# Optimization experiments

Hardware: AMD Instinct MI355X
Metric: run time of the kernel (lower is better)

## Reference

```python
import jax, jax.numpy as jnp
import numpy as np

B, S, E = 2, 2049, 512
H, WIN = 8, 1024
D = E // H


def setup_inputs() -> dict:
    key = jax.random.key(0)
    ks = jax.random.split(key, 11)
    sc = 0.02
    return {
        "x": jax.random.normal(ks[0], (B, S, E), dtype=jnp.float32),
        "Wq": jax.random.normal(ks[1], (E, E), dtype=jnp.float32) * sc,
        "bq": jnp.zeros((E,), dtype=jnp.float32),
        "Wk": jax.random.normal(ks[2], (E, E), dtype=jnp.float32) * sc,
        "bk": jnp.zeros((E,), dtype=jnp.float32),
        "Wv": jax.random.normal(ks[3], (E, E), dtype=jnp.float32) * sc,
        "bv": jnp.zeros((E,), dtype=jnp.float32),
        "Wo": jax.random.normal(ks[4], (E, E), dtype=jnp.float32) * sc,
        "bo": jnp.zeros((E,), dtype=jnp.float32),
        "w_gate": jax.random.normal(ks[5], (2 * E,), dtype=jnp.float32) * sc,
        "b_gate": jnp.zeros((), dtype=jnp.float32),
    }


def reference(x, Wq, bq, Wk, bk, Wv, bv, Wo, bo, w_gate, b_gate):
    scale = D ** -0.5
    q_flat = x @ Wq + bq  # [B,S,E]
    k_flat = x @ Wk + bk
    v_flat = x @ Wv + bv
    q = q_flat.reshape(B, S, H, D).transpose(0, 2, 1, 3)  # [B,H,S,D]
    k = k_flat.reshape(B, S, H, D).transpose(0, 2, 1, 3)
    v = v_flat.reshape(B, S, H, D).transpose(0, 2, 1, 3)

    scores = jnp.einsum("bhqd,bhkd->bhqk", q, k) * scale  # [B,H,S,S]

    # Gaussian positional bias: -0.5*|i-j|^2/sigma^2, sigma = window/2
    pos = jnp.arange(S)
    dist = jnp.abs(pos[:, None] - pos[None, :]).astype(jnp.float32)
    sigma = WIN / 2.0
    bias = -0.5 * dist ** 2 / (sigma ** 2)  # [S,S]
    scores = scores + bias[None, None]

    # Pairwise gate: sigmoid(concat(q_i,k_j) @ w + b) == sigmoid(q_i.wq + k_j.wk + b)
    gq = q_flat @ w_gate[:E]       # [B,S]
    gk = k_flat @ w_gate[E:]       # [B,S]
    gates = jax.nn.sigmoid(gq[:, :, None] + gk[:, None, :] + b_gate)  # [B,S,S]
    scores = scores * gates[:, None]  # broadcast over heads

    local_mask = jnp.where(dist <= WIN, 0.0, -jnp.inf).astype(jnp.float32)
    scores = scores + local_mask[None, None]

    attn = jax.nn.softmax(scores, axis=-1)
    out = jnp.einsum("bhqk,bhkd->bhqd", attn, v)  # [B,H,S,D]
    out = out.transpose(0, 2, 1, 3).reshape(B, S, E)
    return out @ Wo + bo
```

## Files before the change

### kernel.cpp

```cpp
#include <hip/hip_runtime.h>
#include <cstdint>
#include <cstddef>

#define B_ 2
#define S_ 2049
#define E_ 512
#define H_ 8
#define WIN_ 1024
#define MROWS (B_*S_)
#define SP_ 2176
#define GBUFN 4104
#define BHS_ (B_*H_*S_)

typedef unsigned short ushort_t;
typedef __attribute__((ext_vector_type(8))) short bf16x8;
typedef __attribute__((ext_vector_type(4))) float f32x4;

#define MFMA16(a,b,c) __builtin_amdgcn_mfma_f32_16x16x32_bf16(a,b,c,0,0,0)

__device__ __forceinline__ ushort_t f2bf(float f) {
  unsigned int u = __float_as_uint(f);
  u += 0x7fffu + ((u >> 16) & 1u);
  return (ushort_t)(u >> 16);
}
__device__ __forceinline__ float bf2f(ushort_t h) {
  return __uint_as_float(((unsigned int)h) << 16);
}

__global__ __launch_bounds__(256) void convert_w_kernel(
    const float* __restrict__ W0, const float* __restrict__ W1,
    const float* __restrict__ W2, const float* __restrict__ W3,
    ushort_t* __restrict__ Wt_all, ushort_t* __restrict__ WoHi,
    float* __restrict__ gacc)
{
  __shared__ float tile[32][33];
  int z = blockIdx.z;
  if (z == 3) {
    int gz = (blockIdx.x * 16 + blockIdx.y) * 256 + threadIdx.x;
    if (gz < 2 * GBUFN) gacc[gz] = 0.f;
  }
  const float* W = (z == 0) ? W0 : (z == 1) ? W1 : (z == 2) ? W2 : W3;
  int k0 = blockIdx.x * 32, n0 = blockIdx.y * 32;
  int r = threadIdx.x >> 5, c = threadIdx.x & 31;
#pragma unroll
  for (int i = 0; i < 4; ++i) {
    int rr = r + i * 8;
    tile[rr][c] = W[(size_t)(k0 + rr) * E_ + n0 + c];
  }
  __syncthreads();
#pragma unroll
  for (int i = 0; i < 4; ++i) {
    int rr = r + i * 8;
    float v = tile[c][rr];
    size_t dst = (size_t)(n0 + rr) * E_ + k0 + c;
    if (z < 3) Wt_all[(size_t)z * E_ * E_ + dst] = f2bf(v);
    else       WoHi[dst] = f2bf(v);
  }
}

__global__ __launch_bounds__(256) void gemm_qkv_kernel(
    const float* __restrict__ x, const ushort_t* __restrict__ Wt_all,
    const float* __restrict__ bq, const float* __restrict__ bk,
    const float* __restrict__ bv, const float* __restrict__ wg,
    ushort_t* __restrict__ qkb, ushort_t* __restrict__ vT,
    float* __restrict__ gacc)
{
  __shared__ __align__(16) ushort_t As[64][40];
  __shared__ __align__(16) ushort_t Bs[128][40];
  int tid = threadIdx.x;
  int lane = tid & 63, w = tid >> 6;
  int l15 = lane & 15, quad = lane >> 4;
  int wm = (w & 1) * 32, wn = (w >> 1) * 64;
  int z = blockIdx.z;
  const ushort_t* Wt = Wt_all + (size_t)z * E_ * E_;
  const float* bias = (z == 0) ? bq : (z == 1) ? bk : bv;
  int bt = blockIdx.x;
  int bg2 = bt / 33;
  int bm = (bt - bg2 * 33) * 64;
  int bn = blockIdx.y * 128;
  size_t rowbase = (size_t)bg2 * S_;

  int ar = tid >> 2, acq = (tid & 3) * 8;
  int ai = bm + ar; if (ai >= S_) ai = S_ - 1;
  const float* ap = x + (rowbase + ai) * E_ + acq;
  int br = tid >> 1, bcq = (tid & 1) * 16;
  const ushort_t* bp = Wt + (size_t)(bn + br) * E_ + bcq;

  const f32x4 fz = {0.f, 0.f, 0.f, 0.f};
  f32x4 acc[2][4];
#pragma unroll
  for (int mt = 0; mt < 2; ++mt)
#pragma unroll
    for (int nt = 0; nt < 4; ++nt) acc[mt][nt] = fz;

  float4 pa0 = *(const float4*)ap, pa1 = *(const float4*)(ap + 4);
  int4  pb0 = *(const int4*)bp,   pb1 = *(const int4*)(bp + 8);

  for (int k0 = 0; k0 < E_; k0 += 32) {
    __syncthreads();
    int kn = (k0 + 32 < E_) ? (k0 + 32) : k0;
    float4 na0 = *(const float4*)(ap + kn), na1 = *(const float4*)(ap + kn + 4);
    int4  nb0 = *(const int4*)(bp + kn),   nb1 = *(const int4*)(bp + kn + 8);
    union { int4 v; ushort_t u[8]; } cv;
    cv.u[0] = f2bf(pa0.x); cv.u[1] = f2bf(pa0.y); cv.u[2] = f2bf(pa0.z); cv.u[3] = f2bf(pa0.w);
    cv.u[4] = f2bf(pa1.x); cv.u[5] = f2bf(pa1.y); cv.u[6] = f2bf(pa1.z); cv.u[7] = f2bf(pa1.w);
    *(int4*)&As[ar][acq] = cv.v;
    *(int4*)&Bs[br][bcq] = pb0; *(int4*)&Bs[br][bcq + 8] = pb1;
    __syncthreads();
    bf16x8 a[2], bfr[4];
#pragma unroll
    for (int mt = 0; mt < 2; ++mt) a[mt] = *(const bf16x8*)&As[wm + mt * 16 + l15][quad * 8];
#pragma unroll
    for (int nt = 0; nt < 4; ++nt) bfr[nt] = *(const bf16x8*)&Bs[wn + nt * 16 + l15][quad * 8];
#pragma unroll
    for (int mt = 0; mt < 2; ++mt)
#pragma unroll
      for (int nt = 0; nt < 4; ++nt)
        acc[mt][nt] = MFMA16(a[mt], bfr[nt], acc[mt][nt]);
    pa0 = na0; pa1 = na1; pb0 = nb0; pb1 = nb1;
  }

  float bb[4];
#pragma unroll
  for (int nt = 0; nt < 4; ++nt) bb[nt] = bias[bn + wn + nt * 16 + l15];

  if (z < 2) {
    ushort_t* C = qkb + (size_t)z * MROWS * E_;
#pragma unroll
    for (int mt = 0; mt < 2; ++mt)
#pragma unroll
      for (int nt = 0; nt < 4; ++nt)
#pragma unroll
        for (int r = 0; r < 4; ++r) {
          int i = bm + wm + mt * 16 + quad * 4 + r;
          if (i < S_)
            C[(rowbase + i) * E_ + bn + wn + nt * 16 + l15] = f2bf(acc[mt][nt][r] + bb[nt]);
        }
    const float* wgp = wg + (size_t)z * E_;
    float wv[4];
#pragma unroll
    for (int nt = 0; nt < 4; ++nt) wv[nt] = wgp[bn + wn + nt * 16 + l15];
    float* gp = gacc + (size_t)z * GBUFN;
#pragma unroll
    for (int mt = 0; mt < 2; ++mt)
#pragma unroll
      for (int r = 0; r < 4; ++r) {
        float s = 0.f;
#pragma unroll
        for (int nt = 0; nt < 4; ++nt) s = fmaf(acc[mt][nt][r] + bb[nt], wv[nt], s);
        s += __shfl_xor(s, 1, 16); s += __shfl_xor(s, 2, 16);
        s += __shfl_xor(s, 4, 16); s += __shfl_xor(s, 8, 16);
        int i = bm + wm + mt * 16 + quad * 4 + r;
        if (l15 == 0 && i < S_) atomicAdd(&gp[rowbase + i], s);
      }
  } else {
    ushort_t* lt = &Bs[0][0];
    int ti = tid >> 2, tc = (tid & 3) * 16;
#pragma unroll
    for (int hh = 0; hh < 2; ++hh) {
      __syncthreads();
      if ((w >> 1) == hh) {
#pragma unroll
        for (int mt = 0; mt < 2; ++mt)
#pragma unroll
          for (int nt = 0; nt < 4; ++nt) {
            int d = nt * 16 + l15;
#pragma unroll
            for (int r = 0; r < 4; ++r) {
              int il = wm + mt * 16 + quad * 4 + r;
              lt[d * 72 + il] = f2bf(acc[mt][nt][r] + bb[nt]);
            }
          }
      }
      __syncthreads();
      int hg = (bn >> 6) + hh;
      union { int4 q[2]; ushort_t u[16]; } tv;
      tv.q[0] = *(const int4*)&lt[ti * 72 + tc];
      tv.q[1] = *(const int4*)&lt[ti * 72 + tc + 8];
      size_t vrow = ((size_t)(bg2 * H_ + hg) * 64 + ti) * SP_;
#pragma unroll
      for (int c8 = 0; c8 < 2; ++c8) {
        int i2 = bm + tc + c8 * 8;
        if (i2 + 7 < S_) {
          *(int4*)&vT[vrow + i2] = tv.q[c8];
        } else {
#pragma unroll
          for (int e = 0; e < 8; ++e)
            if (i2 + e < S_) vT[vrow + i2 + e] = tv.u[c8 * 8 + e];
        }
      }
    }
  }
}

__global__ __launch_bounds__(256) void attn_kernel(
    const ushort_t* __restrict__ qb, const ushort_t* __restrict__ kb,
    const ushort_t* __restrict__ vT, const float* __restrict__ gq_raw,
    const float* __restrict__ gk_raw, const float* __restrict__ bgate,
    float* __restrict__ Opart, float* __restrict__ Lpart)
{
  __shared__ __align__(16) ushort_t Ks[64][72];
  __shared__ __align__(16) ushort_t Vt[64][72];
  __shared__ __align__(16) ushort_t Ps[4][16][72];
  __shared__ float gbs[704];

  int tid = threadIdx.x;
  int lane = tid & 63, w = tid >> 6;
  int l15 = lane & 15, quad = lane >> 4;

  int sub = blockIdx.x % 48;
  int qidx = blockIdx.x / 48;
  int off = (qidx + 1) >> 1;
  int qt = 16 + ((qidx & 1) ? -off : off);
  int bh = sub & 15, third = sub >> 4;
  int h = bh & 7, b = bh >> 3;
  int i0 = qt * 64;
  const float coef = -0.5f / (512.f * 512.f);

  int i = i0 + w * 16 + l15;
  int ic = (i < S_) ? i : S_ - 1;
  bf16x8 qf0 = *(const bf16x8*)&qb[((size_t)(b * S_ + ic)) * E_ + h * 64 + quad * 8];
  bf16x8 qf1 = *(const bf16x8*)&qb[((size_t)(b * S_ + ic)) * E_ + h * 64 + 32 + quad * 8];
#pragma unroll
  for (int e = 0; e < 8; ++e) {
    qf0[e] = (short)f2bf(bf2f((ushort_t)qf0[e]) * 0.125f);
    qf1[e] = (short)f2bf(bf2f((ushort_t)qf1[e]) * 0.125f);
  }
  float av = __expf(-(gq_raw[b * S_ + ic] + bgate[0]));
  float fdi = (i < S_) ? (float)i : -1e5f;

  int jlo = i0 - WIN_; if (jlo < 0) jlo = 0;
  int jt_lo = jlo >> 6;
  int jhi = i0 + 63 + WIN_; if (jhi > S_ - 1) jhi = S_ - 1;
  int jt_hi = jhi >> 6;
  int L = jt_hi - jt_lo + 1;
  int n0 = (L + 2) / 3, n1 = (L + 1) / 3;
  int myLo = jt_lo + ((third == 0) ? 0 : (third == 1) ? n0 : n0 + n1);
  int cnt = (third == 0) ? n0 : (third == 1) ? n1 : L - n0 - n1;
  int myHi = myLo + cnt - 1;
  int jbase = myLo << 6;
  int nwin = cnt << 6;

  for (int tt = tid; tt < nwin; tt += 256) {
    int j = jbase + tt; int jc = (j < S_) ? j : S_ - 1;
    gbs[tt] = __expf(-gk_raw[b * S_ + jc]);
  }

  int srow = tid >> 2, scol = (tid & 3) * 16;
  const ushort_t* kb_base = kb + (size_t)b * S_ * E_ + h * 64 + scol;
  const ushort_t* vb_base = vT + ((size_t)(b * H_ + h) * 64 + srow) * SP_ + scol;

  int4 ka0, ka1, va0, va1;
  {
    int jc0 = jbase + srow; if (jc0 > S_ - 1) jc0 = S_ - 1;
    const int4* kp = (const int4*)(kb_base + (size_t)jc0 * E_);
    ka0 = kp[0]; ka1 = kp[1];
    const int4* vp = (const int4*)(vb_base + jbase);
    va0 = vp[0]; va1 = vp[1];
  }

  const f32x4 fz = {0.f, 0.f, 0.f, 0.f};
  f32x4 Ov[4] = {fz, fz, fz, fz};
  float l_run = 0.f;

  for (int jt = myLo; jt <= myHi; ++jt) {
    int j0 = jt << 6;
    __syncthreads();
    int jn = (jt < myHi) ? ((jt + 1) << 6) : j0;
    int jcn = jn + srow; if (jcn > S_ - 1) jcn = S_ - 1;
    const int4* kp = (const int4*)(kb_base + (size_t)jcn * E_);
    int4 nk0 = kp[0], nk1 = kp[1];
    const int4* vp = (const int4*)(vb_base + jn);
    int4 nv0 = vp[0], nv1 = vp[1];
    *(int4*)&Ks[srow][scol] = ka0; *(int4*)&Ks[srow][scol + 8] = ka1;
    *(int4*)&Vt[srow][scol] = va0; *(int4*)&Vt[srow][scol + 8] = va1;
    __syncthreads();

    f32x4 st[4];
#pragma unroll
    for (int nt = 0; nt < 4; ++nt) {
      bf16x8 kf0 = *(const bf16x8*)&Ks[nt * 16 + l15][quad * 8];
      bf16x8 kf1 = *(const bf16x8*)&Ks[nt * 16 + l15][32 + quad * 8];
      f32x4 s = MFMA16(kf0, qf0, fz);
      st[nt] = MFMA16(kf1, qf1, s);
    }

    bool full = ((j0 + 63 - i0) <= WIN_) && ((i0 + 63 - j0) <= WIN_)
                && (j0 + 63 < S_) && (i0 + 63 < S_);
    float ps = 0.f;
    float jq = (float)(j0 + quad * 4);
    if (full) {
#pragma unroll
      for (int nt = 0; nt < 4; ++nt) {
        f32x4 g4 = *(const f32x4*)&gbs[(j0 - jbase) + nt * 16 + quad * 4];
#pragma unroll
        for (int r = 0; r < 4; ++r) {
          float f = fdi - (jq + (float)(nt * 16 + r));
          float gate = __builtin_amdgcn_rcpf(fmaf(av, g4[r], 1.f));
          float p = __expf(fmaf(f * f, coef, st[nt][r]) * gate);
          st[nt][r] = p; ps += p;
        }
      }
    } else {
#pragma unroll
      for (int nt = 0; nt < 4; ++nt) {
        f32x4 g4 = *(const f32x4*)&gbs[(j0 - jbase) + nt * 16 + quad * 4];
#pragma unroll
        for (int r = 0; r < 4; ++r) {
          int j = j0 + nt * 16 + quad * 4 + r;
          float fj = (j < S_) ? (float)j : 1e5f;
          float f = fdi - fj;
          float gate = __builtin_amdgcn_rcpf(fmaf(av, g4[r], 1.f));
          float t = fmaf(f * f, coef, st[nt][r]) * gate;
          t = (__builtin_fabsf(f) <= 1024.f) ? t : -1e30f;
          float p = __expf(t);
          st[nt][r] = p; ps += p;
        }
      }
    }
    ps += __shfl_xor(ps, 16);
    ps += __shfl_xor(ps, 32);
    l_run += ps;

#pragma unroll
    for (int nt = 0; nt < 4; ++nt) {
      uint2 pk;
      pk.x = (unsigned int)f2bf(st[nt][0]) | ((unsigned int)f2bf(st[nt][1]) << 16);
      pk.y = (unsigned int)f2bf(st[nt][2]) | ((unsigned int)f2bf(st[nt][3]) << 16);
      *(uint2*)&Ps[w][l15][nt * 16 + quad * 4] = pk;
    }
    bf16x8 p0 = *(const bf16x8*)&Ps[w][l15][quad * 8];
    bf16x8 p1 = *(const bf16x8*)&Ps[w][l15][32 + quad * 8];
#pragma unroll
    for (int nt = 0; nt < 4; ++nt) {
      bf16x8 v0 = *(const bf16x8*)&Vt[nt * 16 + l15][quad * 8];
      bf16x8 v1 = *(const bf16x8*)&Vt[nt * 16 + l15][32 + quad * 8];
      Ov[nt] = MFMA16(p0, v0, Ov[nt]);
      Ov[nt] = MFMA16(p1, v1, Ov[nt]);
    }
    ka0 = nk0; ka1 = nk1; va0 = nv0; va1 = nv1;
  }

  if (lane < 16) {
    int irow = i0 + w * 16 + lane;
    if (irow < S_)
      Lpart[(size_t)third * BHS_ + (size_t)(b * H_ + h) * S_ + irow] = l_run;
  }
#pragma unroll
  for (int r = 0; r < 4; ++r) {
    int irow = i0 + w * 16 + quad * 4 + r;
    if (irow < S_) {
      size_t base = ((size_t)third * BHS_ + (size_t)(b * H_ + h) * S_ + irow) * 64;
#pragma unroll
      for (int nt = 0; nt < 4; ++nt)
        Opart[base + nt * 16 + l15] = Ov[nt][r];
    }
  }
}

__global__ __launch_bounds__(256) void gemm_out_kernel(
    const float* __restrict__ Opart, const float* __restrict__ Lpart,
    const ushort_t* __restrict__ Whi, const float* __restrict__ bias,
    float* __restrict__ C)
{
  __shared__ __align__(16) ushort_t AsH[64][40];
  __shared__ __align__(16) ushort_t AsL[64][40];
  __shared__ __align__(16) ushort_t BsW[64][40];
  __shared__ float invL[64][8];
  int tid = threadIdx.x;
  int lane = tid & 63, w = tid >> 6;
  int l15 = lane & 15, quad = lane >> 4;
  int bm = blockIdx.x * 64, bn = blockIdx.y * 64;

  for (int idx = tid; idx < 512; idx += 256) {
    int r = idx >> 3, hh = idx & 7;
    int m = bm + r; if (m >= MROWS) m = MROWS - 1;
    int b2 = (m >= S_) ? 1 : 0;
    int i = m - b2 * S_;
    size_t li = (size_t)(b2 * H_ + hh) * S_ + i;
    float l = Lpart[li] + Lpart[(size_t)BHS_ + li] + Lpart[2 * (size_t)BHS_ + li];
    invL[r][hh] = 1.f / l;
  }

  int sr = tid >> 2, scq = (tid & 3) * 8;
  int m = bm + sr; if (m >= MROWS) m = MROWS - 1;
  int b2 = (m >= S_) ? 1 : 0;
  int i = m - b2 * S_;
  size_t obase = (((size_t)(b2 * H_) * S_) + i) * 64;
  const ushort_t* bp = Whi + (size_t)(bn + sr) * E_ + scq;

  const f32x4 fz = {0.f, 0.f, 0.f, 0.f};
  f32x4 acc[4] = {fz, fz, fz, fz};
  const size_t TOFF = (size_t)BHS_ * 64;

  for (int k0 = 0; k0 < E_; k0 += 32) {
    __syncthreads();
    int e0 = k0 + scq;
    int h = e0 >> 6, d = e0 & 63;
    const float* op = Opart + obase + (size_t)h * (S_ * 64) + d;
    float4 a0 = *(const float4*)op;
    float4 a1 = *(const float4*)(op + 4);
    float4 q0 = *(const float4*)(op + TOFF);
    float4 q1 = *(const float4*)(op + TOFF + 4);
    float4 c0 = *(const float4*)(op + 2 * TOFF);
    float4 c1 = *(const float4*)(op + 2 * TOFF + 4);
    float sc = invL[sr][h];
    float o[8] = {(a0.x + q0.x + c0.x) * sc, (a0.y + q0.y + c0.y) * sc,
                  (a0.z + q0.z + c0.z) * sc, (a0.w + q0.w + c0.w) * sc,
                  (a1.x + q1.x + c1.x) * sc, (a1.y + q1.y + c1.y) * sc,
                  (a1.z + q1.z + c1.z) * sc, (a1.w + q1.w + c1.w) * sc};
    union { int4 v; ushort_t u[8]; } hi, lo;
#pragma unroll
    for (int e = 0; e < 8; ++e) {
      ushort_t hv = f2bf(o[e]);
      hi.u[e] = hv;
      lo.u[e] = f2bf(o[e] - bf2f(hv));
    }
    *(int4*)&AsH[sr][scq] = hi.v;
    *(int4*)&AsL[sr][scq] = lo.v;
    *(int4*)&BsW[sr][scq] = *(const int4*)(bp + k0);
    __syncthreads();
    bf16x8 ah = *(const bf16x8*)&AsH[w * 16 + l15][quad * 8];
    bf16x8 al = *(const bf16x8*)&AsL[w * 16 + l15][quad * 8];
#pragma unroll
    for (int nt = 0; nt < 4; ++nt) {
      bf16x8 bw = *(const bf16x8*)&BsW[nt * 16 + l15][quad * 8];
      acc[nt] = MFMA16(ah, bw, acc[nt]);
      acc[nt] = MFMA16(al, bw, acc[nt]);
    }
  }
#pragma unroll
  for (int nt = 0; nt < 4; ++nt) {
    float bb = bias[bn + nt * 16 + l15];
#pragma unroll
    for (int r = 0; r < 4; ++r) {
      int mm = bm + w * 16 + quad * 4 + r;
      if (mm < MROWS)
        C[(size_t)mm * E_ + bn + nt * 16 + l15] = acc[nt][r] + bb;
    }
  }
}

extern "C" void kernel_launch(void* const* d_in, const int* in_sizes, int n_in,
                              void* d_out, int out_size, void* d_ws, size_t ws_size,
                              hipStream_t stream) {
  const float* x  = (const float*)d_in[0];
  const float* Wq = (const float*)d_in[1];
  const float* bq = (const float*)d_in[2];
  const float* Wk = (const float*)d_in[3];
  const float* bk = (const float*)d_in[4];
  const float* Wv = (const float*)d_in[5];
  const float* bv = (const float*)d_in[6];
  const float* Wo = (const float*)d_in[7];
  const float* bo = (const float*)d_in[8];
  const float* wg = (const float*)d_in[9];
  const float* bg = (const float*)d_in[10];

  char* p = (char*)d_ws;
  ushort_t* Wt_all = (ushort_t*)p; p += (size_t)3 * E_ * E_ * 2;
  ushort_t* WoHi   = (ushort_t*)p; p += (size_t)E_ * E_ * 2;
  ushort_t* qkb    = (ushort_t*)p; p += (size_t)2 * MROWS * E_ * 2;
  ushort_t* vT     = (ushort_t*)p; p += (size_t)B_ * H_ * 64 * SP_ * 2;
  float*    gacc   = (float*)p;    p += (size_t)2 * GBUFN * 4;
  float*    Opart  = (float*)p;    p += (size_t)3 * BHS_ * 64 * 4;
  float*    Lpart  = (float*)p;    p += (size_t)3 * BHS_ * 4;

  hipLaunchKernelGGL(convert_w_kernel, dim3(16, 16, 4), dim3(256), 0, stream,
                     Wq, Wk, Wv, Wo, Wt_all, WoHi, gacc);
  hipLaunchKernelGGL(gemm_qkv_kernel, dim3(66, 4, 3), dim3(256), 0, stream,
                     x, Wt_all, bq, bk, bv, wg, qkb, vT, gacc);
  hipLaunchKernelGGL(attn_kernel, dim3(33 * 48), dim3(256), 0, stream,
                     qkb, qkb + (size_t)MROWS * E_, vT, gacc, gacc + GBUFN, bg,
                     Opart, Lpart);
  hipLaunchKernelGGL(gemm_out_kernel, dim3(65, 8), dim3(256), 0, stream,
                     Opart, Lpart, WoHi, bo, (float*)d_out);
}
```

Measured before the change: 193.0 us.

## Split split-K combine into separate kernel and prefetch bf16 tiles in output GEMM

Moves the reduction of the three attention partial outputs, the normalization and the hi/lo bf16 split out of the output GEMM into a dedicated combine kernel. That kernel writes bf16 hi/lo activations into the now-free q/k buffer. Previously each of the 8 column blocks of the GEMM recomputed this from fp32 partials, reading the partials eight times over. The GEMM now loads compact bf16 tiles with register prefetch of the next k-step, at the cost of an extra kernel launch and an intermediate write and read.

```diff
diff --git a/kernel.cpp b/kernel.cpp
--- a/kernel.cpp
+++ b/kernel.cpp
@@ -358,67 +358,68 @@
   }
 }
 
+__global__ __launch_bounds__(256) void combine_kernel(
+    const float* __restrict__ Opart, const float* __restrict__ Lpart,
+    ushort_t* __restrict__ ahi, ushort_t* __restrict__ alo)
+{
+  int tid = threadIdx.x;
+  int gi = blockIdx.x * 16 + (tid >> 4);
+  int d4 = tid & 15;
+  int b = gi / (H_ * S_);
+  int rem = gi - b * (H_ * S_);
+  int h = rem / S_;
+  int i = rem - h * S_;
+  size_t p0 = (size_t)(b * H_ + h) * S_ + i;
+  float l = Lpart[p0] + Lpart[p0 + (size_t)BHS_] + Lpart[p0 + 2 * (size_t)BHS_];
+  float inv = 1.f / l;
+  const float* op = Opart + p0 * 64 + d4 * 4;
+  float4 o1 = *(const float4*)op;
+  float4 o2 = *(const float4*)(op + (size_t)BHS_ * 64);
+  float4 o3 = *(const float4*)(op + 2 * (size_t)BHS_ * 64);
+  float o[4] = {(o1.x + o2.x + o3.x) * inv, (o1.y + o2.y + o3.y) * inv,
+                (o1.z + o2.z + o3.z) * inv, (o1.w + o2.w + o3.w) * inv};
+  ushort4 hi, lo;
+  hi.x = f2bf(o[0]); lo.x = f2bf(o[0] - bf2f(hi.x));
+  hi.y = f2bf(o[1]); lo.y = f2bf(o[1] - bf2f(hi.y));
+  hi.z = f2bf(o[2]); lo.z = f2bf(o[2] - bf2f(hi.z));
+  hi.w = f2bf(o[3]); lo.w = f2bf(o[3] - bf2f(hi.w));
+  size_t oidx = ((size_t)b * S_ + i) * E_ + h * 64 + d4 * 4;
+  *(ushort4*)&ahi[oidx] = hi;
+  *(ushort4*)&alo[oidx] = lo;
+}
+
 __global__ __launch_bounds__(256) void gemm_out_kernel(
-    const float* __restrict__ Opart, const float* __restrict__ Lpart,
+    const ushort_t* __restrict__ Ahi, const ushort_t* __restrict__ Alo,
     const ushort_t* __restrict__ Whi, const float* __restrict__ bias,
     float* __restrict__ C)
 {
   __shared__ __align__(16) ushort_t AsH[64][40];
   __shared__ __align__(16) ushort_t AsL[64][40];
   __shared__ __align__(16) ushort_t BsW[64][40];
-  __shared__ float invL[64][8];
   int tid = threadIdx.x;
   int lane = tid & 63, w = tid >> 6;
   int l15 = lane & 15, quad = lane >> 4;
   int bm = blockIdx.x * 64, bn = blockIdx.y * 64;
-
-  for (int idx = tid; idx < 512; idx += 256) {
-    int r = idx >> 3, hh = idx & 7;
-    int m = bm + r; if (m >= MROWS) m = MROWS - 1;
-    int b2 = (m >= S_) ? 1 : 0;
-    int i = m - b2 * S_;
-    size_t li = (size_t)(b2 * H_ + hh) * S_ + i;
-    float l = Lpart[li] + Lpart[(size_t)BHS_ + li] + Lpart[2 * (size_t)BHS_ + li];
-    invL[r][hh] = 1.f / l;
-  }
-
-  int sr = tid >> 2, scq = (tid & 3) * 8;
-  int m = bm + sr; if (m >= MROWS) m = MROWS - 1;
-  int b2 = (m >= S_) ? 1 : 0;
-  int i = m - b2 * S_;
-  size_t obase = (((size_t)(b2 * H_) * S_) + i) * 64;
-  const ushort_t* bp = Whi + (size_t)(bn + sr) * E_ + scq;
+  int sr = tid >> 2, sc = (tid & 3) * 8;
+  int am = bm + sr; if (am >= MROWS) am = MROWS - 1;
+  const ushort_t* ahp = Ahi + (size_t)am * E_ + sc;
+  const ushort_t* alp = Alo + (size_t)am * E_ + sc;
+  const ushort_t* bp  = Whi + (size_t)(bn + sr) * E_ + sc;
 
   const f32x4 fz = {0.f, 0.f, 0.f, 0.f};
   f32x4 acc[4] = {fz, fz, fz, fz};
-  const size_t TOFF = (size_t)BHS_ * 64;
+
+  int4 ph = *(const int4*)ahp, pl = *(const int4*)alp, pb = *(const int4*)bp;
 
   for (int k0 = 0; k0 < E_; k0 += 32) {
     __syncthreads();
-    int e0 = k0 + scq;
-    int h = e0 >> 6, d = e0 & 63;
-    const float* op = Opart + obase + (size_t)h * (S_ * 64) + d;
-    float4 a0 = *(const float4*)op;
-    float4 a1 = *(const float4*)(op + 4);
-    float4 q0 = *(const float4*)(op + TOFF);
-    float4 q1 = *(const float4*)(op + TOFF + 4);
-    float4 c0 = *(const float4*)(op + 2 * TOFF);
-    float4 c1 = *(const float4*)(op + 2 * TOFF + 4);
-    float sc = invL[sr][h];
-    float o[8] = {(a0.x + q0.x + c0.x) * sc, (a0.y + q0.y + c0.y) * sc,
-                  (a0.z + q0.z + c0.z) * sc, (a0.w + q0.w + c0.w) * sc,
-                  (a1.x + q1.x + c1.x) * sc, (a1.y + q1.y + c1.y) * sc,
-                  (a1.z + q1.z + c1.z) * sc, (a1.w + q1.w + c1.w) * sc};
-    union { int4 v; ushort_t u[8]; } hi, lo;
-#pragma unroll
-    for (int e = 0; e < 8; ++e) {
-      ushort_t hv = f2bf(o[e]);
-      hi.u[e] = hv;
-      lo.u[e] = f2bf(o[e] - bf2f(hv));
-    }
-    *(int4*)&AsH[sr][scq] = hi.v;
-    *(int4*)&AsL[sr][scq] = lo.v;
-    *(int4*)&BsW[sr][scq] = *(const int4*)(bp + k0);
+    int kn = (k0 + 32 < E_) ? (k0 + 32) : k0;
+    int4 nh = *(const int4*)(ahp + kn);
+    int4 nl = *(const int4*)(alp + kn);
+    int4 nb = *(const int4*)(bp + kn);
+    *(int4*)&AsH[sr][sc] = ph;
+    *(int4*)&AsL[sr][sc] = pl;
+    *(int4*)&BsW[sr][sc] = pb;
     __syncthreads();
     bf16x8 ah = *(const bf16x8*)&AsH[w * 16 + l15][quad * 8];
     bf16x8 al = *(const bf16x8*)&AsL[w * 16 + l15][quad * 8];
@@ -428,15 +429,16 @@
       acc[nt] = MFMA16(ah, bw, acc[nt]);
       acc[nt] = MFMA16(al, bw, acc[nt]);
     }
+    ph = nh; pl = nl; pb = nb;
   }
 #pragma unroll
   for (int nt = 0; nt < 4; ++nt) {
     float bb = bias[bn + nt * 16 + l15];
 #pragma unroll
     for (int r = 0; r < 4; ++r) {
-      int mm = bm + w * 16 + quad * 4 + r;
-      if (mm < MROWS)
-        C[(size_t)mm * E_ + bn + nt * 16 + l15] = acc[nt][r] + bb;
+      int m = bm + w * 16 + quad * 4 + r;
+      if (m < MROWS)
+        C[(size_t)m * E_ + bn + nt * 16 + l15] = acc[nt][r] + bb;
     }
   }
 }
@@ -464,6 +466,8 @@
   float*    gacc   = (float*)p;    p += (size_t)2 * GBUFN * 4;
   float*    Opart  = (float*)p;    p += (size_t)3 * BHS_ * 64 * 4;
   float*    Lpart  = (float*)p;    p += (size_t)3 * BHS_ * 4;
+  ushort_t* aHi    = qkb;
+  ushort_t* aLo    = qkb + (size_t)MROWS * E_;
 
   hipLaunchKernelGGL(convert_w_kernel, dim3(16, 16, 4), dim3(256), 0, stream,
                      Wq, Wk, Wv, Wo, Wt_all, WoHi, gacc);
@@ -472,6 +476,8 @@
   hipLaunchKernelGGL(attn_kernel, dim3(33 * 48), dim3(256), 0, stream,
                      qkb, qkb + (size_t)MROWS * E_, vT, gacc, gacc + GBUFN, bg,
                      Opart, Lpart);
+  hipLaunchKernelGGL(combine_kernel, dim3(2049), dim3(256), 0, stream,
+                     Opart, Lpart, aHi, aLo);
   hipLaunchKernelGGL(gemm_out_kernel, dim3(65, 8), dim3(256), 0, stream,
-                     Opart, Lpart, WoHi, bo, (float*)d_out);
-}
+                     aHi, aLo, WoHi, bo, (float*)d_out);
+}
```

New measurement: 170.0 us. -11.9%, faster.
